# Kernel optimization log

Hardware: AMD Instinct MI355X
Metric: run time of the kernel (lower is better)

The kernel has to match this reference:

```python
import jax, jax.numpy as jnp
import numpy as np

B, N, CIN, COUT, K, E = 2048, 64, 128, 256, 3, 256
EPS = 1e-5


def setup_inputs() -> dict:
    key = jax.random.key(0)
    ks = jax.random.split(key, 8)
    x = jax.random.normal(ks[0], (B, N, CIN), dtype=jnp.float32)
    edge_index = jax.random.randint(ks[1], (2, E), 0, N, dtype=jnp.int32)
    W = jax.random.normal(ks[2], (CIN, COUT), dtype=jnp.float32) / np.sqrt(CIN)
    b_gcn = jnp.zeros((COUT,), jnp.float32)
    w_conv = jax.random.normal(ks[3], (COUT, COUT, K), dtype=jnp.float32) / np.sqrt(COUT * K)
    b_conv = jnp.zeros((COUT,), jnp.float32)
    gamma = jnp.ones((COUT,), jnp.float32)
    beta = jnp.zeros((COUT,), jnp.float32)
    return {"x": x, "W": W, "b_gcn": b_gcn, "w_conv": w_conv, "b_conv": b_conv,
            "gamma": gamma, "beta": beta, "edge_index": edge_index}


def reference(x, W, b_gcn, w_conv, b_conv, gamma, beta, edge_index):
    Bq, Nn, _ = x.shape
    Co = W.shape[1]
    # ---- GCNConv (PyG semantics: xW, add self-loops, symmetric norm, + bias) ----
    src, dst = edge_index[0], edge_index[1]
    loop = jnp.arange(Nn, dtype=edge_index.dtype)
    src2 = jnp.concatenate([src, loop])           # [E+N]
    dst2 = jnp.concatenate([dst, loop])
    deg = jnp.zeros((Nn,), x.dtype).at[dst2].add(1.0)
    dinv = jnp.where(deg > 0, jax.lax.rsqrt(deg), 0.0)
    norm = dinv[src2] * dinv[dst2]                # [E+N]
    xw = jnp.einsum('bnc,co->bno', x, W)          # [B, N, Co]
    msgs = xw[:, src2, :] * norm[None, :, None]   # [B, E+N, Co]
    x_gcn = jnp.zeros((Bq, Nn, Co), x.dtype).at[:, dst2, :].add(msgs) + b_gcn
    # ---- temporal Conv1d over batch_seq axis, shared weights across nodes ----
    xt = x_gcn.transpose(1, 2, 0)                 # [N, Co, B]  (time = batch_seq)
    pad = K // 2
    y = jax.lax.conv_general_dilated(xt, w_conv, (1,), [(pad, pad)],
                                     dimension_numbers=('NCH', 'OIH', 'NCH'))
    y = y + b_conv[None, :, None]                 # [N, Co, B]
    # ---- BatchNorm1d (training-mode batch stats) + ReLU ----
    y = y.transpose(2, 1, 0)                      # [B, Co, N]
    mean = y.mean(axis=(0, 2), keepdims=True)
    var = ((y - mean) ** 2).mean(axis=(0, 2), keepdims=True)
    y = (y - mean) * jax.lax.rsqrt(var + EPS)
    y = gamma[None, :, None] * y + beta[None, :, None]
    y = jax.nn.relu(y)
    # dropout is identity in eval mode
    return y.transpose(0, 2, 1)                   # [B, N, Co]
```

## Files before the change

### kernel.cpp

```cpp
#include <hip/hip_runtime.h>
#include <hip/hip_bf16.h>

typedef __attribute__((ext_vector_type(8))) unsigned short us8;
typedef __attribute__((ext_vector_type(8))) short short8;
typedef __attribute__((ext_vector_type(4))) float f32x4;

#define BB 2048
#define NN 64
#define CIN 128
#define CO 256
#define KWIN 3
#define EE 256
#define NE 320
#define EPSBN 1e-5f

static __device__ __forceinline__ void gload_lds16(const unsigned short* g, unsigned short* l) {
    __builtin_amdgcn_global_load_lds(
        (const __attribute__((address_space(1))) unsigned int*)g,
        (__attribute__((address_space(3))) unsigned int*)l,
        16, 0, 0);
}

static __device__ __forceinline__ unsigned short f2bfu(float f) {
    unsigned int u = __float_as_uint(f);
    u = (u + 0x7FFFu + ((u >> 16) & 1u)) >> 16;
    return (unsigned short)u;
}

__global__ __launch_bounds__(320) void k_setup(const int* __restrict__ ei,
                                               __hip_bfloat16* __restrict__ Ahat) {
    __shared__ int s_cnt[NN * NN];
    __shared__ int s_deg[NN];
    __shared__ float s_dinv[NN];
    const int t = threadIdx.x;
    for (int i = t; i < NN * NN; i += 320) s_cnt[i] = 0;
    if (t < NN) s_deg[t] = 0;
    __syncthreads();
    int src, dst;
    if (t < EE) { src = ei[t]; dst = ei[EE + t]; }
    else        { src = t - EE; dst = t - EE; }
    atomicAdd(&s_deg[dst], 1);
    atomicAdd(&s_cnt[dst * NN + src], 1);
    __syncthreads();
    if (t < NN) s_dinv[t] = rsqrtf((float)s_deg[t]);
    __syncthreads();
    for (int i = t; i < NN * NN; i += 320) {
        const int n = i >> 6, m = i & 63;
        Ahat[i] = __float2bfloat16((float)s_cnt[i] * s_dinv[m] * s_dinv[n]);
    }
}

__global__ __launch_bounds__(256) void k_wt(const float* __restrict__ W,
                                            __hip_bfloat16* __restrict__ Wt) {
    const int idx = blockIdx.x * 256 + threadIdx.x;
    const int o = idx >> 7, c = idx & 127;
    Wt[idx] = __float2bfloat16(W[c * CO + o]);
}

__global__ __launch_bounds__(256) void k_w2t(const float* __restrict__ wconv,
                                             __hip_bfloat16* __restrict__ W2t) {
    const int idx = blockIdx.x * 256 + threadIdx.x;
    const int o = idx / 768, q = idx - o * 768;
    const int kk = q >> 8, i = q & 255;
    W2t[idx] = __float2bfloat16(wconv[(o * CO + i) * KWIN + kk]);
}

__global__ __launch_bounds__(256) void k_gcn(const float* __restrict__ x,
                                             const __hip_bfloat16* __restrict__ Ahat_,
                                             const __hip_bfloat16* __restrict__ Wt_,
                                             const float* __restrict__ bgcn,
                                             __hip_bfloat16* __restrict__ xgcn_) {
    __shared__ __align__(16) char smem[40960];
    unsigned short* sxT  = (unsigned short*)smem;
    unsigned short* sAh  = (unsigned short*)(smem + 16384);
    unsigned short* stm  = (unsigned short*)(smem + 24576);
    unsigned short* sout = (unsigned short*)smem;
    const unsigned short* Ahat = (const unsigned short*)Ahat_;
    const unsigned short* Wt   = (const unsigned short*)Wt_;
    unsigned short* xgcn = (unsigned short*)xgcn_;

    const int b = blockIdx.x, tid = threadIdx.x;
    const int lane = tid & 63, wid = tid >> 6;
    const int llo = lane & 15, lhi = lane >> 4;

    const float4* xb4 = (const float4*)(x + (size_t)b * NN * CIN);
#pragma unroll
    for (int i = 0; i < 8; ++i) {
        const int f = tid + 256 * i;
        const int m = f >> 5, c0 = (f & 31) * 4;
        const float4 v = xb4[f];
        const float vv[4] = {v.x, v.y, v.z, v.w};
#pragma unroll
        for (int j = 0; j < 4; ++j) {
            const int c = c0 + j;
            sxT[c * 64 + (m ^ ((c & 7) << 3))] = f2bfu(vv[j]);
        }
    }
    {
        const int n = tid >> 2, mb = (tid & 3) * 16;
        const int sw = (n & 7) << 3;
        const us8 a0 = *(const us8*)(Ahat + n * 64 + mb);
        const us8 a1 = *(const us8*)(Ahat + n * 64 + mb + 8);
        *(us8*)&sAh[n * 64 + (mb ^ sw)] = a0;
        *(us8*)&sAh[n * 64 + ((mb + 8) ^ sw)] = a1;
    }
    __syncthreads();

    f32x4 acc1[4][2];
#pragma unroll
    for (int p = 0; p < 4; ++p)
#pragma unroll
        for (int q = 0; q < 2; ++q) acc1[p][q] = (f32x4){0.f, 0.f, 0.f, 0.f};
#pragma unroll
    for (int s = 0; s < 2; ++s) {
        const int k0 = s * 32 + lhi * 8;
        short8 af[4], bf[2];
#pragma unroll
        for (int p = 0; p < 4; ++p) {
            const int n = p * 16 + llo;
            af[p] = *(const short8*)&sAh[n * 64 + (k0 ^ ((n & 7) << 3))];
        }
#pragma unroll
        for (int q = 0; q < 2; ++q) {
            const int c = wid * 32 + q * 16 + llo;
            bf[q] = *(const short8*)&sxT[c * 64 + (k0 ^ ((c & 7) << 3))];
        }
#pragma unroll
        for (int p = 0; p < 4; ++p)
#pragma unroll
            for (int q = 0; q < 2; ++q)
                acc1[p][q] = __builtin_amdgcn_mfma_f32_16x16x32_bf16(af[p], bf[q], acc1[p][q], 0, 0, 0);
    }
#pragma unroll
    for (int p = 0; p < 4; ++p)
#pragma unroll
        for (int q = 0; q < 2; ++q)
#pragma unroll
            for (int reg = 0; reg < 4; ++reg) {
                const int n = p * 16 + lhi * 4 + reg;
                const int c = wid * 32 + q * 16 + llo;
                stm[n * 128 + (c ^ ((n & 7) << 3))] = f2bfu(acc1[p][q][reg]);
            }
    __syncthreads();

    f32x4 acc2[4][4];
#pragma unroll
    for (int p = 0; p < 4; ++p)
#pragma unroll
        for (int q = 0; q < 4; ++q) acc2[p][q] = (f32x4){0.f, 0.f, 0.f, 0.f};
#pragma unroll
    for (int s = 0; s < 4; ++s) {
        const int k0 = s * 32 + lhi * 8;
        short8 af[4], bf[4];
#pragma unroll
        for (int p = 0; p < 4; ++p) {
            const int n = p * 16 + llo;
            af[p] = *(const short8*)&stm[n * 128 + (k0 ^ ((n & 7) << 3))];
        }
#pragma unroll
        for (int q = 0; q < 4; ++q) {
            const int o = wid * 64 + q * 16 + llo;
            bf[q] = *(const short8*)&Wt[o * 128 + k0];
        }
#pragma unroll
        for (int p = 0; p < 4; ++p)
#pragma unroll
            for (int q = 0; q < 4; ++q)
                acc2[p][q] = __builtin_amdgcn_mfma_f32_16x16x32_bf16(af[p], bf[q], acc2[p][q], 0, 0, 0);
    }
    __syncthreads();

    float bg[4];
#pragma unroll
    for (int q = 0; q < 4; ++q) bg[q] = bgcn[wid * 64 + q * 16 + llo];
#pragma unroll
    for (int p = 0; p < 4; ++p)
#pragma unroll
        for (int q = 0; q < 4; ++q)
#pragma unroll
            for (int reg = 0; reg < 4; ++reg) {
                const int n = p * 16 + lhi * 4 + reg;
                const int o = wid * 64 + q * 16 + llo;
                sout[n * 256 + o] = f2bfu(acc2[p][q][reg] + bg[q]);
            }
    __syncthreads();
    unsigned short* dst = xgcn + (size_t)b * NN * CO;
#pragma unroll
    for (int i = 0; i < 8; ++i) {
        const int f = tid + 256 * i;
        *(us8*)(dst + f * 8) = *(const us8*)&sout[f * 8];
    }
}

__global__ __launch_bounds__(256) void k_conv(const __hip_bfloat16* __restrict__ xgcn_,
                                              const __hip_bfloat16* __restrict__ W2t_,
                                              const float* __restrict__ bconv,
                                              float* __restrict__ y,
                                              float* __restrict__ partials) {
    __shared__ unsigned short sA[128 * 64];
    __shared__ unsigned short sB[128 * 64];
    const unsigned short* xgcn = (const unsigned short*)xgcn_;
    const unsigned short* W2t  = (const unsigned short*)W2t_;

    const int tt = blockIdx.x, ot = blockIdx.y, n = blockIdx.z;
    const int tid = threadIdx.x;
    const int lane = tid & 63, wid = tid >> 6;
    const int t0 = tt * 128, o0 = ot * 128;
    const int wm0 = (wid >> 1) * 64, wn0 = (wid & 1) * 64;
    const int lhi = lane >> 4, llo = lane & 15;

    f32x4 acc[4][4];
#pragma unroll
    for (int m = 0; m < 4; ++m)
#pragma unroll
        for (int nn = 0; nn < 4; ++nn) acc[m][nn] = (f32x4){0.f, 0.f, 0.f, 0.f};

    const int srsub = lane >> 3;
    const int scol  = (((lane & 7) ^ srsub) << 3);

    for (int kc = 0; kc < 12; ++kc) {
        const int kk = kc >> 2;
        const int i0 = (kc & 3) * 64;
        const int q0 = kc * 64;
#pragma unroll
        for (int iss = 0; iss < 4; ++iss) {
            const int row = wid * 32 + iss * 8 + srsub;
            int tg = t0 + row + kk - 1;
            tg = min(max(tg, 0), BB - 1);
            gload_lds16(xgcn + ((size_t)tg * NN + n) * CO + i0 + scol,
                        sA + (wid * 32 + iss * 8) * 64);
        }
#pragma unroll
        for (int iss = 0; iss < 4; ++iss) {
            const int row = wid * 32 + iss * 8 + srsub;
            gload_lds16(W2t + (size_t)(o0 + row) * (CO * KWIN) + q0 + scol,
                        sB + (wid * 32 + iss * 8) * 64);
        }
        __syncthreads();
        if ((tt == 0 && kc < 4) || (tt == 15 && kc >= 8)) {
            const int zr = (tt == 0) ? 0 : 127;
            if (tid < 8) *(uint4*)&sA[zr * 64 + tid * 8] = make_uint4(0u, 0u, 0u, 0u);
            __syncthreads();
        }
#pragma unroll
        for (int s = 0; s < 2; ++s) {
            const int cu = s * 32 + lhi * 8;
            short8 af[4], bf[4];
#pragma unroll
            for (int m = 0; m < 4; ++m) {
                const int row = wm0 + m * 16 + llo;
                af[m] = *(const short8*)&sA[row * 64 + (cu ^ ((row & 7) << 3))];
            }
#pragma unroll
            for (int nn = 0; nn < 4; ++nn) {
                const int row = wn0 + nn * 16 + llo;
                bf[nn] = *(const short8*)&sB[row * 64 + (cu ^ ((row & 7) << 3))];
            }
#pragma unroll
            for (int m = 0; m < 4; ++m)
#pragma unroll
                for (int nn = 0; nn < 4; ++nn)
                    acc[m][nn] = __builtin_amdgcn_mfma_f32_16x16x32_bf16(af[m], bf[nn], acc[m][nn], 0, 0, 0);
        }
        __syncthreads();
    }

    float bc[4], s1v[4], s2v[4];
#pragma unroll
    for (int nn = 0; nn < 4; ++nn) {
        bc[nn] = bconv[o0 + wn0 + nn * 16 + llo];
        s1v[nn] = 0.f; s2v[nn] = 0.f;
    }
#pragma unroll
    for (int m = 0; m < 4; ++m) {
#pragma unroll
        for (int reg = 0; reg < 4; ++reg) {
            const int trow = t0 + wm0 + m * 16 + lhi * 4 + reg;
            float* dst = y + ((size_t)trow * NN + n) * CO + o0 + wn0 + llo;
#pragma unroll
            for (int nn = 0; nn < 4; ++nn) {
                const float v = acc[m][nn][reg] + bc[nn];
                dst[nn * 16] = v;
                s1v[nn] += v;
                s2v[nn] += v * v;
            }
        }
    }
    float* sred1 = (float*)sA;
    float* sred2 = sred1 + 1024;
    const int rg = (wid >> 1) * 4 + lhi;
#pragma unroll
    for (int nn = 0; nn < 4; ++nn) {
        const int cl = wn0 + nn * 16 + llo;
        sred1[rg * 128 + cl] = s1v[nn];
        sred2[rg * 128 + cl] = s2v[nn];
    }
    __syncthreads();
    if (tid < 128) {
        float a = 0.f, b2 = 0.f;
#pragma unroll
        for (int r = 0; r < 8; ++r) { a += sred1[r * 128 + tid]; b2 += sred2[r * 128 + tid]; }
        float* pb = partials + (size_t)((n * 2 + ot) * 16 + tt) * 256;
        pb[tid * 2]     = a;
        pb[tid * 2 + 1] = b2;
    }
}

__global__ __launch_bounds__(256) void k_bnstats(const float* __restrict__ partials,
                                                 const float* __restrict__ gamma,
                                                 const float* __restrict__ beta,
                                                 float* __restrict__ scl,
                                                 float* __restrict__ shf) {
    const int o = blockIdx.x, tid = threadIdx.x;
    const int ot = o >> 7, c = o & 127;
    float s1 = 0.f, s2 = 0.f;
    for (int i = tid; i < 1024; i += 256) {
        const int nn = i >> 4, tt = i & 15;
        const float* p = partials + ((size_t)((nn * 2 + ot) * 16 + tt)) * 256 + c * 2;
        s1 += p[0]; s2 += p[1];
    }
    __shared__ float r1[256], r2[256];
    r1[tid] = s1; r2[tid] = s2;
    __syncthreads();
    for (int s = 128; s > 0; s >>= 1) {
        if (tid < s) { r1[tid] += r1[tid + s]; r2[tid] += r2[tid + s]; }
        __syncthreads();
    }
    if (tid == 0) {
        const float inv = 1.f / (float)((size_t)BB * NN);
        const float mean = r1[0] * inv;
        const float var  = r2[0] * inv - mean * mean;
        const float sc = gamma[o] * rsqrtf(var + EPSBN);
        scl[o] = sc;
        shf[o] = beta[o] - mean * sc;
    }
}

__global__ __launch_bounds__(256) void k_apply(float* __restrict__ y,
                                               const float* __restrict__ scl,
                                               const float* __restrict__ shf) {
    __shared__ float ssc[CO], ssh[CO];
    const int tid = threadIdx.x;
    ssc[tid] = scl[tid]; ssh[tid] = shf[tid];
    __syncthreads();
    const size_t total4 = (size_t)BB * NN * CO / 4;
    float4* y4 = (float4*)y;
    for (size_t i = (size_t)blockIdx.x * 256 + tid; i < total4; i += (size_t)gridDim.x * 256) {
        float4 v = y4[i];
        const int ob = (int)((i * 4) & (CO - 1));
        v.x = fmaxf(0.f, v.x * ssc[ob]     + ssh[ob]);
        v.y = fmaxf(0.f, v.y * ssc[ob + 1] + ssh[ob + 1]);
        v.z = fmaxf(0.f, v.z * ssc[ob + 2] + ssh[ob + 2]);
        v.w = fmaxf(0.f, v.w * ssc[ob + 3] + ssh[ob + 3]);
        y4[i] = v;
    }
}

extern "C" void kernel_launch(void* const* d_in, const int* in_sizes, int n_in,
                              void* d_out, int out_size, void* d_ws, size_t ws_size,
                              hipStream_t stream) {
    const float* x     = (const float*)d_in[0];
    const float* W     = (const float*)d_in[1];
    const float* bgcn  = (const float*)d_in[2];
    const float* wconv = (const float*)d_in[3];
    const float* bconv = (const float*)d_in[4];
    const float* gamma = (const float*)d_in[5];
    const float* beta  = (const float*)d_in[6];
    const int*   ei    = (const int*)d_in[7];
    float* out = (float*)d_out;

    char* ws = (char*)d_ws;
    size_t off = 0;
    __hip_bfloat16* xgcn = (__hip_bfloat16*)(ws + off); off += (size_t)BB * NN * CO * 2;
    __hip_bfloat16* W2t  = (__hip_bfloat16*)(ws + off); off += (size_t)CO * KWIN * CO * 2;
    __hip_bfloat16* Ahat = (__hip_bfloat16*)(ws + off); off += (size_t)NN * NN * 2;
    __hip_bfloat16* Wt   = (__hip_bfloat16*)(ws + off); off += (size_t)CO * CIN * 2;
    float* partials = (float*)(ws + off); off += (size_t)2048 * 256 * 4;
    float* scl = (float*)(ws + off); off += 256 * 4;
    float* shf = (float*)(ws + off); off += 256 * 4;

    k_setup<<<1, 320, 0, stream>>>(ei, Ahat);
    k_wt<<<128, 256, 0, stream>>>(W, Wt);
    k_w2t<<<768, 256, 0, stream>>>(wconv, W2t);
    k_gcn<<<BB, 256, 0, stream>>>(x, Ahat, Wt, bgcn, xgcn);
    k_conv<<<dim3(16, 2, 64), 256, 0, stream>>>(xgcn, W2t, bconv, out, partials);
    k_bnstats<<<256, 256, 0, stream>>>(partials, gamma, beta, scl, shf);
    k_apply<<<2048, 256, 0, stream>>>(out, scl, shf);
}
```

Before: 167.5 us.

## Reorder GCN matmuls, reuse conv input tile across taps, store intermediate in bf16

The GCN kernel now computes x·W first and then applies Ahat, reading x row-major and Ahat directly from global memory. The temporal conv loads one 130-row input tile per channel chunk and reuses it for all three taps, double-buffering the weight slices instead of reloading activations per tap. The pre-BN conv output is written as bf16 to a workspace buffer, and the apply pass reads bf16 and writes fp32, roughly halving intermediate traffic. The two weight-prep kernels are merged into one launch. The bf16 intermediate adds rounding error before normalization.

```diff
diff --git a/kernel.cpp b/kernel.cpp
--- a/kernel.cpp
+++ b/kernel.cpp
@@ -2,6 +2,7 @@
 #include <hip/hip_bf16.h>
 
 typedef __attribute__((ext_vector_type(8))) unsigned short us8;
+typedef __attribute__((ext_vector_type(4))) unsigned short us4;
 typedef __attribute__((ext_vector_type(8))) short short8;
 typedef __attribute__((ext_vector_type(4))) float f32x4;
 
@@ -21,6 +22,10 @@
         16, 0, 0);
 }
 
+static __device__ __forceinline__ float bf2f(unsigned short u) {
+    return __uint_as_float(((unsigned int)u) << 16);
+}
+
 static __device__ __forceinline__ unsigned short f2bfu(float f) {
     unsigned int u = __float_as_uint(f);
     u = (u + 0x7FFFu + ((u >> 16) & 1u)) >> 16;
@@ -50,19 +55,21 @@
     }
 }
 
-__global__ __launch_bounds__(256) void k_wt(const float* __restrict__ W,
-                                            __hip_bfloat16* __restrict__ Wt) {
+__global__ __launch_bounds__(256) void k_weights(const float* __restrict__ W,
+                                                 const float* __restrict__ wconv,
+                                                 __hip_bfloat16* __restrict__ Wt,
+                                                 __hip_bfloat16* __restrict__ W2t) {
     const int idx = blockIdx.x * 256 + threadIdx.x;
-    const int o = idx >> 7, c = idx & 127;
-    Wt[idx] = __float2bfloat16(W[c * CO + o]);
-}
-
-__global__ __launch_bounds__(256) void k_w2t(const float* __restrict__ wconv,
-                                             __hip_bfloat16* __restrict__ W2t) {
-    const int idx = blockIdx.x * 256 + threadIdx.x;
-    const int o = idx / 768, q = idx - o * 768;
-    const int kk = q >> 8, i = q & 255;
-    W2t[idx] = __float2bfloat16(wconv[(o * CO + i) * KWIN + kk]);
+    if (idx < CO * CIN) {
+        const int o = idx >> 7, c = idx & 127;
+        Wt[idx] = __float2bfloat16(W[c * CO + o]);
+    }
+    const int j = idx - CO * CIN;
+    if (j >= 0 && j < CO * KWIN * CO) {
+        const int o = j / 768, q = j - o * 768;
+        const int kk = q >> 8, i = q & 255;
+        W2t[j] = __float2bfloat16(wconv[(o * CO + i) * KWIN + kk]);
+    }
 }
 
 __global__ __launch_bounds__(256) void k_gcn(const float* __restrict__ x,
@@ -70,11 +77,8 @@
                                              const __hip_bfloat16* __restrict__ Wt_,
                                              const float* __restrict__ bgcn,
                                              __hip_bfloat16* __restrict__ xgcn_) {
-    __shared__ __align__(16) char smem[40960];
-    unsigned short* sxT  = (unsigned short*)smem;
-    unsigned short* sAh  = (unsigned short*)(smem + 16384);
-    unsigned short* stm  = (unsigned short*)(smem + 24576);
-    unsigned short* sout = (unsigned short*)smem;
+    __shared__ __align__(16) unsigned short sx[64 * 128];
+    __shared__ __align__(16) unsigned short stm[256 * 64];
     const unsigned short* Ahat = (const unsigned short*)Ahat_;
     const unsigned short* Wt   = (const unsigned short*)Wt_;
     unsigned short* xgcn = (unsigned short*)xgcn_;
@@ -83,79 +87,31 @@
     const int lane = tid & 63, wid = tid >> 6;
     const int llo = lane & 15, lhi = lane >> 4;
 
-    const float4* xb4 = (const float4*)(x + (size_t)b * NN * CIN);
-#pragma unroll
-    for (int i = 0; i < 8; ++i) {
-        const int f = tid + 256 * i;
-        const int m = f >> 5, c0 = (f & 31) * 4;
-        const float4 v = xb4[f];
-        const float vv[4] = {v.x, v.y, v.z, v.w};
-#pragma unroll
-        for (int j = 0; j < 4; ++j) {
-            const int c = c0 + j;
-            sxT[c * 64 + (m ^ ((c & 7) << 3))] = f2bfu(vv[j]);
-        }
-    }
-    {
-        const int n = tid >> 2, mb = (tid & 3) * 16;
-        const int sw = (n & 7) << 3;
-        const us8 a0 = *(const us8*)(Ahat + n * 64 + mb);
-        const us8 a1 = *(const us8*)(Ahat + n * 64 + mb + 8);
-        *(us8*)&sAh[n * 64 + (mb ^ sw)] = a0;
-        *(us8*)&sAh[n * 64 + ((mb + 8) ^ sw)] = a1;
-    }
-    __syncthreads();
-
-    f32x4 acc1[4][2];
+#pragma unroll
+    for (int r = 0; r < 4; ++r) {
+        const int f = tid + 256 * r;
+        const int m = f >> 4, c0 = (f & 15) * 8;
+        const float4* src = (const float4*)(x + ((size_t)b * NN + m) * CIN + c0);
+        const float4 v0 = src[0], v1 = src[1];
+        unsigned short t8[8] = {f2bfu(v0.x), f2bfu(v0.y), f2bfu(v0.z), f2bfu(v0.w),
+                                f2bfu(v1.x), f2bfu(v1.y), f2bfu(v1.z), f2bfu(v1.w)};
+        *(us8*)&sx[m * 128 + (c0 ^ ((m & 7) << 3))] = *(const us8*)t8;
+    }
+    __syncthreads();
+
+    f32x4 acc1[4][4];
 #pragma unroll
     for (int p = 0; p < 4; ++p)
 #pragma unroll
-        for (int q = 0; q < 2; ++q) acc1[p][q] = (f32x4){0.f, 0.f, 0.f, 0.f};
-#pragma unroll
-    for (int s = 0; s < 2; ++s) {
-        const int k0 = s * 32 + lhi * 8;
-        short8 af[4], bf[2];
-#pragma unroll
-        for (int p = 0; p < 4; ++p) {
-            const int n = p * 16 + llo;
-            af[p] = *(const short8*)&sAh[n * 64 + (k0 ^ ((n & 7) << 3))];
-        }
-#pragma unroll
-        for (int q = 0; q < 2; ++q) {
-            const int c = wid * 32 + q * 16 + llo;
-            bf[q] = *(const short8*)&sxT[c * 64 + (k0 ^ ((c & 7) << 3))];
-        }
-#pragma unroll
-        for (int p = 0; p < 4; ++p)
-#pragma unroll
-            for (int q = 0; q < 2; ++q)
-                acc1[p][q] = __builtin_amdgcn_mfma_f32_16x16x32_bf16(af[p], bf[q], acc1[p][q], 0, 0, 0);
-    }
-#pragma unroll
-    for (int p = 0; p < 4; ++p)
-#pragma unroll
-        for (int q = 0; q < 2; ++q)
-#pragma unroll
-            for (int reg = 0; reg < 4; ++reg) {
-                const int n = p * 16 + lhi * 4 + reg;
-                const int c = wid * 32 + q * 16 + llo;
-                stm[n * 128 + (c ^ ((n & 7) << 3))] = f2bfu(acc1[p][q][reg]);
-            }
-    __syncthreads();
-
-    f32x4 acc2[4][4];
-#pragma unroll
-    for (int p = 0; p < 4; ++p)
-#pragma unroll
-        for (int q = 0; q < 4; ++q) acc2[p][q] = (f32x4){0.f, 0.f, 0.f, 0.f};
+        for (int q = 0; q < 4; ++q) acc1[p][q] = (f32x4){0.f, 0.f, 0.f, 0.f};
 #pragma unroll
     for (int s = 0; s < 4; ++s) {
         const int k0 = s * 32 + lhi * 8;
         short8 af[4], bf[4];
 #pragma unroll
         for (int p = 0; p < 4; ++p) {
-            const int n = p * 16 + llo;
-            af[p] = *(const short8*)&stm[n * 128 + (k0 ^ ((n & 7) << 3))];
+            const int m = p * 16 + llo;
+            af[p] = *(const short8*)&sx[m * 128 + (k0 ^ ((m & 7) << 3))];
         }
 #pragma unroll
         for (int q = 0; q < 4; ++q) {
@@ -166,41 +122,72 @@
         for (int p = 0; p < 4; ++p)
 #pragma unroll
             for (int q = 0; q < 4; ++q)
+                acc1[p][q] = __builtin_amdgcn_mfma_f32_16x16x32_bf16(af[p], bf[q], acc1[p][q], 0, 0, 0);
+    }
+#pragma unroll
+    for (int p = 0; p < 4; ++p)
+#pragma unroll
+        for (int q = 0; q < 4; ++q) {
+            const int o = wid * 64 + q * 16 + llo;
+            const int bm = p * 16 + lhi * 4;
+            unsigned short t4[4] = {f2bfu(acc1[p][q][0]), f2bfu(acc1[p][q][1]),
+                                    f2bfu(acc1[p][q][2]), f2bfu(acc1[p][q][3])};
+            *(us4*)&stm[o * 64 + (bm ^ ((o & 7) << 3))] = *(const us4*)t4;
+        }
+
+    f32x4 acc2[4][4];
+#pragma unroll
+    for (int p = 0; p < 4; ++p)
+#pragma unroll
+        for (int q = 0; q < 4; ++q) acc2[p][q] = (f32x4){0.f, 0.f, 0.f, 0.f};
+#pragma unroll
+    for (int s = 0; s < 2; ++s) {
+        const int k0 = s * 32 + lhi * 8;
+        short8 af[4], bf[4];
+#pragma unroll
+        for (int p = 0; p < 4; ++p) {
+            const int n = p * 16 + llo;
+            af[p] = *(const short8*)&Ahat[n * 64 + k0];
+        }
+#pragma unroll
+        for (int q = 0; q < 4; ++q) {
+            const int o = wid * 64 + q * 16 + llo;
+            bf[q] = *(const short8*)&stm[o * 64 + (k0 ^ ((o & 7) << 3))];
+        }
+#pragma unroll
+        for (int p = 0; p < 4; ++p)
+#pragma unroll
+            for (int q = 0; q < 4; ++q)
                 acc2[p][q] = __builtin_amdgcn_mfma_f32_16x16x32_bf16(af[p], bf[q], acc2[p][q], 0, 0, 0);
     }
-    __syncthreads();
 
     float bg[4];
 #pragma unroll
     for (int q = 0; q < 4; ++q) bg[q] = bgcn[wid * 64 + q * 16 + llo];
+    unsigned short* dst = xgcn + (size_t)b * NN * CO;
 #pragma unroll
     for (int p = 0; p < 4; ++p)
 #pragma unroll
-        for (int q = 0; q < 4; ++q)
+        for (int q = 0; q < 4; ++q) {
+            const int o = wid * 64 + q * 16 + llo;
 #pragma unroll
             for (int reg = 0; reg < 4; ++reg) {
                 const int n = p * 16 + lhi * 4 + reg;
-                const int o = wid * 64 + q * 16 + llo;
-                sout[n * 256 + o] = f2bfu(acc2[p][q][reg] + bg[q]);
+                dst[n * CO + o] = f2bfu(acc2[p][q][reg] + bg[q]);
             }
-    __syncthreads();
-    unsigned short* dst = xgcn + (size_t)b * NN * CO;
-#pragma unroll
-    for (int i = 0; i < 8; ++i) {
-        const int f = tid + 256 * i;
-        *(us8*)(dst + f * 8) = *(const us8*)&sout[f * 8];
-    }
+        }
 }
 
 __global__ __launch_bounds__(256) void k_conv(const __hip_bfloat16* __restrict__ xgcn_,
                                               const __hip_bfloat16* __restrict__ W2t_,
                                               const float* __restrict__ bconv,
-                                              float* __restrict__ y,
+                                              __hip_bfloat16* __restrict__ y_,
                                               float* __restrict__ partials) {
-    __shared__ unsigned short sA[128 * 64];
-    __shared__ unsigned short sB[128 * 64];
+    __shared__ __align__(16) unsigned short sA[136 * 64];
+    __shared__ __align__(16) unsigned short sB[2][128 * 64];
     const unsigned short* xgcn = (const unsigned short*)xgcn_;
     const unsigned short* W2t  = (const unsigned short*)W2t_;
+    unsigned short* y = (unsigned short*)y_;
 
     const int tt = blockIdx.x, ot = blockIdx.y, n = blockIdx.z;
     const int tid = threadIdx.x;
@@ -218,51 +205,59 @@
     const int srsub = lane >> 3;
     const int scol  = (((lane & 7) ^ srsub) << 3);
 
-    for (int kc = 0; kc < 12; ++kc) {
-        const int kk = kc >> 2;
-        const int i0 = (kc & 3) * 64;
-        const int q0 = kc * 64;
+    for (int g = 0; g < 4; ++g) {
+        const int i0 = g * 64;
+        for (int iss = wid; iss < 17; iss += 4) {
+            const int rbase = iss * 8;
+            int tg = t0 - 1 + rbase + srsub;
+            tg = min(max(tg, 0), BB - 1);
+            gload_lds16(xgcn + ((size_t)tg * NN + n) * CO + i0 + scol, sA + rbase * 64);
+        }
 #pragma unroll
         for (int iss = 0; iss < 4; ++iss) {
-            const int row = wid * 32 + iss * 8 + srsub;
-            int tg = t0 + row + kk - 1;
-            tg = min(max(tg, 0), BB - 1);
-            gload_lds16(xgcn + ((size_t)tg * NN + n) * CO + i0 + scol,
-                        sA + (wid * 32 + iss * 8) * 64);
-        }
-#pragma unroll
-        for (int iss = 0; iss < 4; ++iss) {
-            const int row = wid * 32 + iss * 8 + srsub;
-            gload_lds16(W2t + (size_t)(o0 + row) * (CO * KWIN) + q0 + scol,
-                        sB + (wid * 32 + iss * 8) * 64);
+            const int rbase = wid * 32 + iss * 8;
+            gload_lds16(W2t + (size_t)(o0 + rbase + srsub) * (CO * KWIN) + i0 + scol,
+                        sB[0] + rbase * 64);
         }
         __syncthreads();
-        if ((tt == 0 && kc < 4) || (tt == 15 && kc >= 8)) {
-            const int zr = (tt == 0) ? 0 : 127;
+        if (tt == 0 || tt == 15) {
+            const int zr = (tt == 0) ? 0 : 129;
             if (tid < 8) *(uint4*)&sA[zr * 64 + tid * 8] = make_uint4(0u, 0u, 0u, 0u);
             __syncthreads();
         }
 #pragma unroll
-        for (int s = 0; s < 2; ++s) {
-            const int cu = s * 32 + lhi * 8;
-            short8 af[4], bf[4];
-#pragma unroll
-            for (int m = 0; m < 4; ++m) {
-                const int row = wm0 + m * 16 + llo;
-                af[m] = *(const short8*)&sA[row * 64 + (cu ^ ((row & 7) << 3))];
+        for (int kk = 0; kk < 3; ++kk) {
+            if (kk < 2) {
+                const int q0 = (kk + 1) * 256 + i0;
+#pragma unroll
+                for (int iss = 0; iss < 4; ++iss) {
+                    const int rbase = wid * 32 + iss * 8;
+                    gload_lds16(W2t + (size_t)(o0 + rbase + srsub) * (CO * KWIN) + q0 + scol,
+                                sB[(kk + 1) & 1] + rbase * 64);
+                }
             }
 #pragma unroll
-            for (int nn = 0; nn < 4; ++nn) {
-                const int row = wn0 + nn * 16 + llo;
-                bf[nn] = *(const short8*)&sB[row * 64 + (cu ^ ((row & 7) << 3))];
+            for (int s = 0; s < 2; ++s) {
+                const int cu = s * 32 + lhi * 8;
+                short8 af[4], bf[4];
+#pragma unroll
+                for (int m = 0; m < 4; ++m) {
+                    const int sr = wm0 + m * 16 + llo + kk;
+                    af[m] = *(const short8*)&sA[sr * 64 + (cu ^ ((sr & 7) << 3))];
+                }
+#pragma unroll
+                for (int nn = 0; nn < 4; ++nn) {
+                    const int row = wn0 + nn * 16 + llo;
+                    bf[nn] = *(const short8*)&sB[kk & 1][row * 64 + (cu ^ ((row & 7) << 3))];
+                }
+#pragma unroll
+                for (int m = 0; m < 4; ++m)
+#pragma unroll
+                    for (int nn = 0; nn < 4; ++nn)
+                        acc[m][nn] = __builtin_amdgcn_mfma_f32_16x16x32_bf16(af[m], bf[nn], acc[m][nn], 0, 0, 0);
             }
-#pragma unroll
-            for (int m = 0; m < 4; ++m)
-#pragma unroll
-                for (int nn = 0; nn < 4; ++nn)
-                    acc[m][nn] = __builtin_amdgcn_mfma_f32_16x16x32_bf16(af[m], bf[nn], acc[m][nn], 0, 0, 0);
-        }
-        __syncthreads();
+            __syncthreads();
+        }
     }
 
     float bc[4], s1v[4], s2v[4];
@@ -276,11 +271,11 @@
 #pragma unroll
         for (int reg = 0; reg < 4; ++reg) {
             const int trow = t0 + wm0 + m * 16 + lhi * 4 + reg;
-            float* dst = y + ((size_t)trow * NN + n) * CO + o0 + wn0 + llo;
+            unsigned short* dst = y + ((size_t)trow * NN + n) * CO + o0 + wn0 + llo;
 #pragma unroll
             for (int nn = 0; nn < 4; ++nn) {
                 const float v = acc[m][nn][reg] + bc[nn];
-                dst[nn * 16] = v;
+                dst[nn * 16] = f2bfu(v);
                 s1v[nn] += v;
                 s2v[nn] += v * v;
             }
@@ -336,23 +331,30 @@
     }
 }
 
-__global__ __launch_bounds__(256) void k_apply(float* __restrict__ y,
+__global__ __launch_bounds__(256) void k_apply(const unsigned short* __restrict__ y,
+                                               float* __restrict__ out,
                                                const float* __restrict__ scl,
                                                const float* __restrict__ shf) {
     __shared__ float ssc[CO], ssh[CO];
     const int tid = threadIdx.x;
     ssc[tid] = scl[tid]; ssh[tid] = shf[tid];
     __syncthreads();
-    const size_t total4 = (size_t)BB * NN * CO / 4;
-    float4* y4 = (float4*)y;
-    for (size_t i = (size_t)blockIdx.x * 256 + tid; i < total4; i += (size_t)gridDim.x * 256) {
-        float4 v = y4[i];
-        const int ob = (int)((i * 4) & (CO - 1));
-        v.x = fmaxf(0.f, v.x * ssc[ob]     + ssh[ob]);
-        v.y = fmaxf(0.f, v.y * ssc[ob + 1] + ssh[ob + 1]);
-        v.z = fmaxf(0.f, v.z * ssc[ob + 2] + ssh[ob + 2]);
-        v.w = fmaxf(0.f, v.w * ssc[ob + 3] + ssh[ob + 3]);
-        y4[i] = v;
+    const size_t total8 = (size_t)BB * NN * CO / 8;
+    float4* out4 = (float4*)out;
+    for (size_t i = (size_t)blockIdx.x * 256 + tid; i < total8; i += (size_t)gridDim.x * 256) {
+        const us8 v = *(const us8*)(y + i * 8);
+        const int ob = (int)((i * 8) & (CO - 1));
+        float4 r0, r1;
+        r0.x = fmaxf(0.f, bf2f(v[0]) * ssc[ob + 0] + ssh[ob + 0]);
+        r0.y = fmaxf(0.f, bf2f(v[1]) * ssc[ob + 1] + ssh[ob + 1]);
+        r0.z = fmaxf(0.f, bf2f(v[2]) * ssc[ob + 2] + ssh[ob + 2]);
+        r0.w = fmaxf(0.f, bf2f(v[3]) * ssc[ob + 3] + ssh[ob + 3]);
+        r1.x = fmaxf(0.f, bf2f(v[4]) * ssc[ob + 4] + ssh[ob + 4]);
+        r1.y = fmaxf(0.f, bf2f(v[5]) * ssc[ob + 5] + ssh[ob + 5]);
+        r1.z = fmaxf(0.f, bf2f(v[6]) * ssc[ob + 6] + ssh[ob + 6]);
+        r1.w = fmaxf(0.f, bf2f(v[7]) * ssc[ob + 7] + ssh[ob + 7]);
+        out4[i * 2]     = r0;
+        out4[i * 2 + 1] = r1;
     }
 }
 
@@ -372,6 +374,7 @@
     char* ws = (char*)d_ws;
     size_t off = 0;
     __hip_bfloat16* xgcn = (__hip_bfloat16*)(ws + off); off += (size_t)BB * NN * CO * 2;
+    __hip_bfloat16* ybuf = (__hip_bfloat16*)(ws + off); off += (size_t)BB * NN * CO * 2;
     __hip_bfloat16* W2t  = (__hip_bfloat16*)(ws + off); off += (size_t)CO * KWIN * CO * 2;
     __hip_bfloat16* Ahat = (__hip_bfloat16*)(ws + off); off += (size_t)NN * NN * 2;
     __hip_bfloat16* Wt   = (__hip_bfloat16*)(ws + off); off += (size_t)CO * CIN * 2;
@@ -380,10 +383,9 @@
     float* shf = (float*)(ws + off); off += 256 * 4;
 
     k_setup<<<1, 320, 0, stream>>>(ei, Ahat);
-    k_wt<<<128, 256, 0, stream>>>(W, Wt);
-    k_w2t<<<768, 256, 0, stream>>>(wconv, W2t);
+    k_weights<<<896, 256, 0, stream>>>(W, wconv, Wt, W2t);
     k_gcn<<<BB, 256, 0, stream>>>(x, Ahat, Wt, bgcn, xgcn);
-    k_conv<<<dim3(16, 2, 64), 256, 0, stream>>>(xgcn, W2t, bconv, out, partials);
+    k_conv<<<dim3(16, 2, 64), 256, 0, stream>>>(xgcn, W2t, bconv, ybuf, partials);
     k_bnstats<<<256, 256, 0, stream>>>(partials, gamma, beta, scl, shf);
-    k_apply<<<2048, 256, 0, stream>>>(out, scl, shf);
-}
+    k_apply<<<2048, 256, 0, stream>>>((const unsigned short*)ybuf, out, scl, shf);
+}
```

New measurement: 156.2 us. -6.7%, faster.
